# Optimization experiments

Measured on AMD Instinct MI355X. Metric: run time of the kernel, lower is better.

Reference implementation:

```python
import jax, jax.numpy as jnp
import numpy as np

NUM_EMBEDDINGS = 1024
EMBEDDING_DIM = 64
COMMITMENT_COST = 0.25


def setup_inputs() -> dict:
    key = jax.random.key(0)
    k1, k2 = jax.random.split(key)
    inputs = jax.random.normal(k1, (64, 32, 32, EMBEDDING_DIM), dtype=jnp.float32)
    embeddings = jax.random.normal(k2, (NUM_EMBEDDINGS, EMBEDDING_DIM), dtype=jnp.float32)
    return {"inputs": inputs, "embeddings": embeddings}


def reference(inputs, embeddings):
    # flatten spatial dims: [B, HW, D]
    flat = jnp.reshape(inputs, (inputs.shape[0], -1, EMBEDDING_DIM))
    distances = (
        jnp.sum(flat ** 2, axis=2, keepdims=True)
        - 2.0 * jnp.einsum("btd,kd->btk", flat, embeddings)
        + jnp.sum(embeddings ** 2, axis=1)
    )
    encoding_indices = jnp.argmin(distances, axis=2)  # [B, HW]
    # direct gather == one-hot @ embeddings, same math, no [B,HW,K] one-hot
    quantized = jnp.take(embeddings, encoding_indices, axis=0)  # [B, HW, D]
    quantized = jnp.reshape(quantized, inputs.shape)
    e_latent_loss = jnp.mean((jax.lax.stop_gradient(quantized) - inputs) ** 2)
    loss = COMMITMENT_COST * e_latent_loss
    quantized = inputs + jax.lax.stop_gradient(quantized - inputs)
    return quantized, loss, encoding_indices
```

## Files before the change

### kernel.cpp

```cpp
#include <hip/hip_runtime.h>

#define D 64
#define NK 1024
#define QTOTAL 65536
#define NELEM (QTOTAL * D)
#define LOSS_OFF 4194304
#define IDX_OUT_OFF 4194305
#define CAPQ 16384
#define MARGIN 2.0e-3f

typedef float f32x16 __attribute__((ext_vector_type(16)));
typedef short bf16x8 __attribute__((ext_vector_type(8)));
typedef float f32x4 __attribute__((ext_vector_type(4)));
typedef float f32x2 __attribute__((ext_vector_type(2)));
typedef unsigned int u32;
typedef unsigned short ushort_t;

#define WS_E2   0
#define WS_B    4096
#define WS_CNT  266240
#define WS_LIST 266496
#define WS_NEED 332032

__device__ __forceinline__ ushort_t f2bf(float f) {
    u32 u = __float_as_uint(f);
    return (ushort_t)((u + 0x7FFFu + ((u >> 16) & 1u)) >> 16);
}
__device__ __forceinline__ float bf2f(ushort_t h) {
    return __uint_as_float(((u32)h) << 16);
}

__global__ __launch_bounds__(256) void vqk0(const float* __restrict__ emb,
                                            u32* __restrict__ b32,
                                            float* __restrict__ e2, u32* __restrict__ cnt,
                                            float* __restrict__ out) {
    int gid = blockIdx.x * 256 + threadIdx.x;
    int c = gid >> 5;
    int d = (gid & 31) * 2;
    float2 v = ((const float2*)emb)[gid];
    ushort_t h0 = f2bf(v.x), h1 = f2bf(v.y);
    ushort_t m0 = f2bf(v.x - bf2f(h0)), m1 = f2bf(v.y - bf2f(h1));
    int t = c >> 4, row = c & 15;
    int g = (d & 31) >> 3;
    int bh = (d < 32) ? 0 : 1;
    int lane = g * 16 + row;
    int u = t * 1024 + lane * 4 + ((d & 7) >> 1);
    b32[u + bh * 256]       = (u32)h0 | ((u32)h1 << 16);
    b32[u + (bh + 2) * 256] = (u32)m0 | ((u32)m1 << 16);
    if (gid < NK) {
        const float4* e4 = (const float4*)(emb + (long)gid * D);
        float s = 0.f;
#pragma unroll
        for (int i = 0; i < D / 4; ++i) {
            float4 w = e4[i];
            s += w.x * w.x + w.y * w.y + w.z * w.z + w.w * w.w;
        }
        e2[gid] = s;
    }
    if (gid == 0) { out[LOSS_OFF] = 0.0f; *cnt = 0; }
}

#define COMPUTE_TILE(T, BH0, BH1, BM0, BM1) do {                               \
    const int c_ = (T) * 16 + row;                                             \
    const float h_ = e2l[c_];                                                  \
    f32x4 acc = {0.f, 0.f, 0.f, 0.f};                                          \
    acc = __builtin_amdgcn_mfma_f32_16x16x32_bf16(ah[0], BM0, acc, 0, 0, 0);   \
    acc = __builtin_amdgcn_mfma_f32_16x16x32_bf16(am[0], BH0, acc, 0, 0, 0);   \
    acc = __builtin_amdgcn_mfma_f32_16x16x32_bf16(ah[0], BH0, acc, 0, 0, 0);   \
    acc = __builtin_amdgcn_mfma_f32_16x16x32_bf16(ah[1], BM1, acc, 0, 0, 0);   \
    acc = __builtin_amdgcn_mfma_f32_16x16x32_bf16(am[1], BH1, acc, 0, 0, 0);   \
    acc = __builtin_amdgcn_mfma_f32_16x16x32_bf16(ah[1], BH1, acc, 0, 0, 0);   \
    _Pragma("unroll")                                                          \
    for (int r_ = 0; r_ < 4; ++r_) {                                           \
        float sd_ = h_ - acc[r_];                                              \
        float ns2_ = fminf(fmaxf(sd_, s1v[r_]), s2v[r_]);            \
        bool lt_ = sd_ < s1v[r_];                                              \
        i1v[r_] = lt_ ? c_ : i1v[r_];                                          \
        s1v[r_] = fminf(sd_, s1v[r_]);                                         \
        s2v[r_] = ns2_;                                                        \
    }                                                                          \
} while (0)

#define LDS_FRAG(SB, TT, H0, H1, M0, M1) do {                                  \
    const ushort_t* p_ = (SB) + (TT) * 2048 + l * 8;                           \
    H0 = *(const bf16x8*)(p_);                                                 \
    H1 = *(const bf16x8*)(p_ + 512);                                           \
    M0 = *(const bf16x8*)(p_ + 1024);                                          \
    M1 = *(const bf16x8*)(p_ + 1536);                                          \
} while (0)

__global__ __launch_bounds__(512, 4) void vqk1(const float* __restrict__ x,
                                               const ushort_t* __restrict__ B,
                                               const float* __restrict__ e2g,
                                               const float* __restrict__ emb,
                                               u32* __restrict__ cnt,
                                               int* __restrict__ list,
                                               float* __restrict__ out) {
    __shared__ f32x4 stage[2][2048];
    __shared__ float e2l[NK];
    __shared__ int   idx_l[128];
    __shared__ float lred[8];

    const int tid = threadIdx.x;
    const int l = tid & 63;
    const int w = tid >> 6;
    const int qbase = blockIdx.x * 128;
    const int wb = qbase + w * 16;
    const int row = l & 15;
    const int g = l >> 4;
    const int koff = g * 8;

    {
        f32x2 t = ((const f32x2*)e2g)[tid];
        ((f32x2*)e2l)[tid] = t * 0.5f;
    }

    bf16x8 ah[2], am[2];
    {
        const float* xr = x + (long)(wb + row) * D + koff;
#pragma unroll
        for (int half = 0; half < 2; ++half) {
            float4 p0 = ((const float4*)(xr + half * 32))[0];
            float4 p1 = ((const float4*)(xr + half * 32))[1];
            float v[8] = {p0.x, p0.y, p0.z, p0.w, p1.x, p1.y, p1.z, p1.w};
#pragma unroll
            for (int i = 0; i < 8; ++i) {
                ushort_t hs = f2bf(v[i]);
                ushort_t ms = f2bf(v[i] - bf2f(hs));
                ah[half][i] = (short)hs;
                am[half][i] = (short)ms;
            }
        }
    }

    float s1v[4], s2v[4];
    int i1v[4];
#pragma unroll
    for (int i = 0; i < 4; ++i) { s1v[i] = 3.4e38f; s2v[i] = 3.4e38f; i1v[i] = 0; }

    const f32x4* gB = (const f32x4*)B;

    {
        f32x4 st0[4];
#pragma unroll
        for (int tt = 0; tt < 4; ++tt) st0[tt] = gB[tt * 512 + tid];
#pragma unroll
        for (int tt = 0; tt < 4; ++tt) stage[0][tt * 512 + tid] = st0[tt];
    }
    __syncthreads();

#pragma unroll 1
    for (int c = 0; c < 8; ++c) {
        const int cb = c & 1;
        const ushort_t* sb = (const ushort_t*)&stage[cb][0];

        f32x4 st[4];
        if (c < 7) {
#pragma unroll
            for (int tt = 0; tt < 4; ++tt)
                st[tt] = gB[(c + 1) * 2048 + tt * 512 + tid];
        }

        bf16x8 bh0, bh1, bm0, bm1, nh0, nh1, nm0, nm1;
        LDS_FRAG(sb, 0, bh0, bh1, bm0, bm1);
#pragma unroll
        for (int tt = 0; tt < 8; ++tt) {
            if (tt < 7) LDS_FRAG(sb, tt + 1, nh0, nh1, nm0, nm1);
            COMPUTE_TILE(c * 8 + tt, bh0, bh1, bm0, bm1);
            bh0 = nh0; bh1 = nh1; bm0 = nm0; bm1 = nm1;
        }

        if (c < 7) {
#pragma unroll
            for (int tt = 0; tt < 4; ++tt)
                stage[cb ^ 1][tt * 512 + tid] = st[tt];
        }
        __syncthreads();
    }

#pragma unroll
    for (int d = 1; d < 16; d <<= 1) {
#pragma unroll
        for (int sl = 0; sl < 4; ++sl) {
            float os1 = __shfl_xor(s1v[sl], d, 64);
            float os2 = __shfl_xor(s2v[sl], d, 64);
            int   oi1 = __shfl_xor(i1v[sl], d, 64);
            float hi = s1v[sl] > os1 ? s1v[sl] : os1;
            float lo2 = s2v[sl] < os2 ? s2v[sl] : os2;
            int ni = (os1 < s1v[sl]) ? oi1
                   : ((os1 == s1v[sl] && oi1 < i1v[sl]) ? oi1 : i1v[sl]);
            s1v[sl] = s1v[sl] < os1 ? s1v[sl] : os1;
            s2v[sl] = hi < lo2 ? hi : lo2;
            i1v[sl] = ni;
        }
    }

    if (row == 0) {
#pragma unroll
        for (int sl = 0; sl < 4; ++sl) {
            int ql = w * 16 + g * 4 + sl;
            idx_l[ql] = i1v[sl];
            if (s2v[sl] - s1v[sl] <= MARGIN) {
                u32 p = atomicAdd(cnt, 1u);
                if (p < CAPQ) list[p] = qbase + ql;
            }
        }
    }
    __syncthreads();

    if (l < 16) out[IDX_OUT_OFF + wb + l] = (float)idx_l[w * 16 + l];

    const f32x4* x4 = (const f32x4*)(x + (long)wb * D);
    const f32x4* e4 = (const f32x4*)emb;
    f32x4* o4 = (f32x4*)(out + (long)wb * D);
    float ls = 0.f;
#pragma unroll 1
    for (int k = 0; k < 4; ++k) {
        int j = l + 64 * k;
        int ql = j >> 4;
        int col = j & 15;
        int idx = idx_l[w * 16 + ql];
        f32x4 xv = x4[j];
        f32x4 ev = e4[idx * 16 + col];
        o4[j] = ev;
        f32x4 dd = ev - xv;
        ls += dd[0] * dd[0] + dd[1] * dd[1] + dd[2] * dd[2] + dd[3] * dd[3];
    }
#pragma unroll
    for (int offr = 32; offr > 0; offr >>= 1) ls += __shfl_down(ls, offr, 64);
    if (l == 0) lred[w] = ls;
    __syncthreads();
    if (tid == 0) {
        float t = 0.f;
#pragma unroll
        for (int i = 0; i < 8; ++i) t += lred[i];
        atomicAdd(&out[LOSS_OFF], t * (0.25f / (float)NELEM));
    }
}

__global__ __launch_bounds__(64) void vqk2(const float* __restrict__ x,
                                           const float* __restrict__ emb,
                                           const float* __restrict__ e2,
                                           const int* __restrict__ list,
                                           const u32* __restrict__ cnt,
                                           float* __restrict__ out) {
    u32 n = *cnt; if (n > CAPQ) n = CAPQ;
    const int l = threadIdx.x;
    for (u32 f = blockIdx.x; f < n; f += gridDim.x) {
        int q = list[f];
        float4 xv[16];
        const float4* xp = (const float4*)(x + (long)q * D);
#pragma unroll
        for (int i = 0; i < 16; ++i) xv[i] = xp[i];
        float best = 3.4e38f; int bi = 0;
#pragma unroll 1
        for (int i = 0; i < 16; ++i) {
            int c = l * 16 + i;
            const float4* ep = (const float4*)(emb + (long)c * D);
            float a0 = 0.f, a1 = 0.f, a2 = 0.f, a3 = 0.f;
#pragma unroll
            for (int k = 0; k < 16; ++k) {
                float4 e = ep[k];
                a0 = fmaf(e.x, xv[k].x, a0); a1 = fmaf(e.y, xv[k].y, a1);
                a2 = fmaf(e.z, xv[k].z, a2); a3 = fmaf(e.w, xv[k].w, a3);
            }
            float s = 0.5f * e2[c] - ((a0 + a1) + (a2 + a3));
            if (s < best) { best = s; bi = c; }
        }
#pragma unroll
        for (int off = 32; off > 0; off >>= 1) {
            float ob = __shfl_down(best, off, 64);
            int   oi = __shfl_down(bi, off, 64);
            if (ob < best || (ob == best && oi < bi)) { best = ob; bi = oi; }
        }
        bi = __shfl(bi, 0, 64);
        int ci = (int)out[IDX_OUT_OFF + q];
        if (bi != ci) {
            float xl = x[(long)q * D + l];
            float en = emb[(long)bi * D + l];
            float eo = emb[(long)ci * D + l];
            out[(long)q * D + l] = en;
            float dn = (en - xl) * (en - xl);
            float dol = (eo - xl) * (eo - xl);
            float dd = dn - dol;
#pragma unroll
            for (int off = 32; off > 0; off >>= 1) dd += __shfl_down(dd, off, 64);
            if (l == 0) {
                out[IDX_OUT_OFF + q] = (float)bi;
                atomicAdd(&out[LOSS_OFF], dd * (0.25f / (float)NELEM));
            }
        }
    }
}

#define FDO_CHUNK(B, K) \
    aA0 = fmaf(B[0],  xA[4*K+0].x, aA0); aA1 = fmaf(B[1],  xA[4*K+0].y, aA1); \
    aA2 = fmaf(B[2],  xA[4*K+0].z, aA2); aA3 = fmaf(B[3],  xA[4*K+0].w, aA3); \
    aA0 = fmaf(B[4],  xA[4*K+1].x, aA0); aA1 = fmaf(B[5],  xA[4*K+1].y, aA1); \
    aA2 = fmaf(B[6],  xA[4*K+1].z, aA2); aA3 = fmaf(B[7],  xA[4*K+1].w, aA3); \
    aA0 = fmaf(B[8],  xA[4*K+2].x, aA0); aA1 = fmaf(B[9],  xA[4*K+2].y, aA1); \
    aA2 = fmaf(B[10], xA[4*K+2].z, aA2); aA3 = fmaf(B[11], xA[4*K+2].w, aA3); \
    aA0 = fmaf(B[12], xA[4*K+3].x, aA0); aA1 = fmaf(B[13], xA[4*K+3].y, aA1); \
    aA2 = fmaf(B[14], xA[4*K+3].z, aA2); aA3 = fmaf(B[15], xA[4*K+3].w, aA3); \
    aB0 = fmaf(B[0],  xB[4*K+0].x, aB0); aB1 = fmaf(B[1],  xB[4*K+0].y, aB1); \
    aB2 = fmaf(B[2],  xB[4*K+0].z, aB2); aB3 = fmaf(B[3],  xB[4*K+0].w, aB3); \
    aB0 = fmaf(B[4],  xB[4*K+1].x, aB0); aB1 = fmaf(B[5],  xB[4*K+1].y, aB1); \
    aB2 = fmaf(B[6],  xB[4*K+1].z, aB2); aB3 = fmaf(B[7],  xB[4*K+1].w, aB3); \
    aB0 = fmaf(B[8],  xB[4*K+2].x, aB0); aB1 = fmaf(B[9],  xB[4*K+2].y, aB1); \
    aB2 = fmaf(B[10], xB[4*K+2].z, aB2); aB3 = fmaf(B[11], xB[4*K+2].w, aB3); \
    aB0 = fmaf(B[12], xB[4*K+3].x, aB0); aB1 = fmaf(B[13], xB[4*K+3].y, aB1); \
    aB2 = fmaf(B[14], xB[4*K+3].z, aB2); aB3 = fmaf(B[15], xB[4*K+3].w, aB3);

__global__ __launch_bounds__(256) void vq_e2f(const float* __restrict__ emb,
                                              float* __restrict__ e2,
                                              float* __restrict__ out) {
    int k = blockIdx.x * blockDim.x + threadIdx.x;
    if (k == 0) out[LOSS_OFF] = 0.0f;
    if (k < NK) {
        const float4* e4 = (const float4*)(emb + k * D);
        float s = 0.f;
#pragma unroll
        for (int i = 0; i < D / 4; ++i) {
            float4 v = e4[i];
            s += v.x * v.x + v.y * v.y + v.z * v.z + v.w * v.w;
        }
        e2[k] = s;
    }
}

__global__ __launch_bounds__(256, 2) void vq_mainf(const float* __restrict__ x,
                                                   const float* __restrict__ emb,
                                                   const float* __restrict__ e2g,
                                                   float* __restrict__ out) {
    __shared__ float e2l[NK];
    __shared__ float sm_s[512];
    __shared__ int   sm_c[512];
    const int tid = threadIdx.x;
    const int l = tid & 63;
    const int w = tid >> 6;
    const int qbase = blockIdx.x * 128;
    ((float4*)e2l)[tid] = ((const float4*)e2g)[tid];
    float4 xA[16], xB[16];
    const float4* xpA = (const float4*)(x + (long)(qbase + l) * D);
    const float4* xpB = (const float4*)(x + (long)(qbase + 64 + l) * D);
#pragma unroll
    for (int i = 0; i < 16; ++i) { xA[i] = xpA[i]; xB[i] = xpB[i]; }
    __syncthreads();
    const int code0 = __builtin_amdgcn_readfirstlane(w << 8);
    const float* ep0 = emb + (long)code0 * D;
    float bestA = 3.4e38f, bestB = 3.4e38f;
    int idxA = 0, idxB = 0;
#pragma unroll 1
    for (int g = 0; g < 256; ++g) {
        const float* ep = ep0 + g * D;
        f32x16 b0, b1, b2, b3;
        asm volatile(
            "s_load_dwordx16 %0, %4, 0x0\n\t"
            "s_load_dwordx16 %1, %4, 0x40\n\t"
            "s_load_dwordx16 %2, %4, 0x80\n\t"
            "s_load_dwordx16 %3, %4, 0xC0\n\t"
            "s_waitcnt lgkmcnt(0)"
            : "=s"(b0), "=s"(b1), "=s"(b2), "=s"(b3) : "s"(ep));
        float aA0 = 0.f, aA1 = 0.f, aA2 = 0.f, aA3 = 0.f;
        float aB0 = 0.f, aB1 = 0.f, aB2 = 0.f, aB3 = 0.f;
        FDO_CHUNK(b0, 0) FDO_CHUNK(b1, 1) FDO_CHUNK(b2, 2) FDO_CHUNK(b3, 3)
        float dotA = (aA0 + aA1) + (aA2 + aA3);
        float dotB = (aB0 + aB1) + (aB2 + aB3);
        float e2c = e2l[code0 + g];
        float sA = 0.5f * e2c - dotA;
        float sB = 0.5f * e2c - dotB;
        int code = code0 + g;
        bool lt;
        lt = sA < bestA; bestA = lt ? sA : bestA; idxA = lt ? code : idxA;
        lt = sB < bestB; bestB = lt ? sB : bestB; idxB = lt ? code : idxB;
    }
    sm_s[w * 128 + l] = bestA;      sm_c[w * 128 + l] = idxA;
    sm_s[w * 128 + 64 + l] = bestB; sm_c[w * 128 + 64 + l] = idxB;
    __syncthreads();
    if (tid < 128) {
        float bs = sm_s[tid]; int bc = sm_c[tid];
#pragma unroll
        for (int wv = 1; wv < 4; ++wv) {
            float s = sm_s[wv * 128 + tid]; int c = sm_c[wv * 128 + tid];
            if (s < bs) { bs = s; bc = c; }
        }
        const int q = qbase + tid;
        out[IDX_OUT_OFF + q] = (float)bc;
        const float4* eb = (const float4*)(emb + (long)bc * D);
        const float4* xq = (const float4*)(x + (long)q * D);
        float4* oq = (float4*)(out + (long)q * D);
        float lsum = 0.f;
#pragma unroll
        for (int i = 0; i < 16; ++i) {
            float4 e = eb[i]; float4 xx = xq[i];
            oq[i] = e;
            float dx = e.x - xx.x, dy = e.y - xx.y, dz = e.z - xx.z, dw = e.w - xx.w;
            lsum += dx * dx + dy * dy + dz * dz + dw * dw;
        }
#pragma unroll
        for (int o = 32; o > 0; o >>= 1) lsum += __shfl_down(lsum, o, 64);
        if ((tid & 63) == 0) atomicAdd(&out[LOSS_OFF], lsum * (0.25f / (float)NELEM));
    }
}

extern "C" void kernel_launch(void* const* d_in, const int* in_sizes, int n_in,
                              void* d_out, int out_size, void* d_ws, size_t ws_size,
                              hipStream_t stream) {
    const float* x   = (const float*)d_in[0];
    const float* emb = (const float*)d_in[1];
    float* out = (float*)d_out;
    char* ws = (char*)d_ws;

    if (ws_size < (size_t)WS_NEED) {
        float* e2 = (float*)ws;
        vq_e2f<<<4, 256, 0, stream>>>(emb, e2, out);
        vq_mainf<<<QTOTAL / 128, 256, 0, stream>>>(x, emb, e2, out);
        return;
    }

    float* e2    = (float*)(ws + WS_E2);
    ushort_t* B  = (ushort_t*)(ws + WS_B);
    u32* cnt     = (u32*)(ws + WS_CNT);
    int* list    = (int*)(ws + WS_LIST);

    vqk0<<<128, 256, 0, stream>>>(emb, (u32*)B, e2, cnt, out);
    vqk1<<<QTOTAL / 128, 512, 0, stream>>>(x, B, e2, emb, cnt, list, out);
    vqk2<<<256, 64, 0, stream>>>(x, emb, e2, list, cnt, out);
}
```

Before: 121.0 us.

## Stream codebook via direct global-to-LDS loads, halve block size, split MFMA chains

```diff
diff --git a/kernel.cpp b/kernel.cpp
--- a/kernel.cpp
+++ b/kernel.cpp
@@ -12,7 +12,6 @@
 typedef float f32x16 __attribute__((ext_vector_type(16)));
 typedef short bf16x8 __attribute__((ext_vector_type(8)));
 typedef float f32x4 __attribute__((ext_vector_type(4)));
-typedef float f32x2 __attribute__((ext_vector_type(2)));
 typedef unsigned int u32;
 typedef unsigned short ushort_t;
 
@@ -29,6 +28,14 @@
 __device__ __forceinline__ float bf2f(ushort_t h) {
     return __uint_as_float(((u32)h) << 16);
 }
+
+#define GL2LDS(G, L)                                                           \
+    __builtin_amdgcn_global_load_lds(                                          \
+        (const __attribute__((address_space(1))) void*)                        \
+            (unsigned long long)(const void*)(G),                              \
+        (__attribute__((address_space(3))) void*)                              \
+            (unsigned)(unsigned long long)(const void*)(L),                    \
+        16, 0, 0)
 
 __global__ __launch_bounds__(256) void vqk0(const float* __restrict__ emb,
                                             u32* __restrict__ b32,
@@ -63,16 +70,17 @@
 #define COMPUTE_TILE(T, BH0, BH1, BM0, BM1) do {                               \
     const int c_ = (T) * 16 + row;                                             \
     const float h_ = e2l[c_];                                                  \
-    f32x4 acc = {0.f, 0.f, 0.f, 0.f};                                          \
-    acc = __builtin_amdgcn_mfma_f32_16x16x32_bf16(ah[0], BM0, acc, 0, 0, 0);   \
-    acc = __builtin_amdgcn_mfma_f32_16x16x32_bf16(am[0], BH0, acc, 0, 0, 0);   \
-    acc = __builtin_amdgcn_mfma_f32_16x16x32_bf16(ah[0], BH0, acc, 0, 0, 0);   \
-    acc = __builtin_amdgcn_mfma_f32_16x16x32_bf16(ah[1], BM1, acc, 0, 0, 0);   \
-    acc = __builtin_amdgcn_mfma_f32_16x16x32_bf16(am[1], BH1, acc, 0, 0, 0);   \
-    acc = __builtin_amdgcn_mfma_f32_16x16x32_bf16(ah[1], BH1, acc, 0, 0, 0);   \
+    f32x4 a0 = {0.f, 0.f, 0.f, 0.f};                                           \
+    f32x4 a1 = {0.f, 0.f, 0.f, 0.f};                                           \
+    a0 = __builtin_amdgcn_mfma_f32_16x16x32_bf16(ah[0], BM0, a0, 0, 0, 0);     \
+    a1 = __builtin_amdgcn_mfma_f32_16x16x32_bf16(ah[1], BM1, a1, 0, 0, 0);     \
+    a0 = __builtin_amdgcn_mfma_f32_16x16x32_bf16(am[0], BH0, a0, 0, 0, 0);     \
+    a1 = __builtin_amdgcn_mfma_f32_16x16x32_bf16(am[1], BH1, a1, 0, 0, 0);     \
+    a0 = __builtin_amdgcn_mfma_f32_16x16x32_bf16(ah[0], BH0, a0, 0, 0, 0);     \
+    a1 = __builtin_amdgcn_mfma_f32_16x16x32_bf16(ah[1], BH1, a1, 0, 0, 0);     \
     _Pragma("unroll")                                                          \
     for (int r_ = 0; r_ < 4; ++r_) {                                           \
-        float sd_ = h_ - acc[r_];                                              \
+        float sd_ = h_ - a0[r_] - a1[r_];                                      \
         float ns2_ = fminf(fmaxf(sd_, s1v[r_]), s2v[r_]);            \
         bool lt_ = sd_ < s1v[r_];                                              \
         i1v[r_] = lt_ ? c_ : i1v[r_];                                          \
@@ -89,30 +97,35 @@
     M1 = *(const bf16x8*)(p_ + 1536);                                          \
 } while (0)
 
-__global__ __launch_bounds__(512, 4) void vqk1(const float* __restrict__ x,
+__global__ __launch_bounds__(256, 4) void vqk1(const float* __restrict__ x,
                                                const ushort_t* __restrict__ B,
                                                const float* __restrict__ e2g,
                                                const float* __restrict__ emb,
                                                u32* __restrict__ cnt,
                                                int* __restrict__ list,
                                                float* __restrict__ out) {
-    __shared__ f32x4 stage[2][2048];
+    __shared__ f32x4 stage[2][1024];
     __shared__ float e2l[NK];
-    __shared__ int   idx_l[128];
-    __shared__ float lred[8];
+    __shared__ int   idx_l[64];
+    __shared__ float lred[4];
 
     const int tid = threadIdx.x;
     const int l = tid & 63;
     const int w = tid >> 6;
-    const int qbase = blockIdx.x * 128;
+    const int qbase = blockIdx.x * 64;
     const int wb = qbase + w * 16;
     const int row = l & 15;
     const int g = l >> 4;
     const int koff = g * 8;
 
+    const f32x4* gB = (const f32x4*)B;
+
+#pragma unroll
+    for (int tt = 0; tt < 4; ++tt)
+        GL2LDS(gB + tt * 256 + tid, &stage[0][tt * 256 + (tid & 192)]);
     {
-        f32x2 t = ((const f32x2*)e2g)[tid];
-        ((f32x2*)e2l)[tid] = t * 0.5f;
+        f32x4 t = ((const f32x4*)e2g)[tid];
+        ((f32x4*)e2l)[tid] = t * 0.5f;
     }
 
     bf16x8 ah[2], am[2];
@@ -138,42 +151,27 @@
 #pragma unroll
     for (int i = 0; i < 4; ++i) { s1v[i] = 3.4e38f; s2v[i] = 3.4e38f; i1v[i] = 0; }
 
-    const f32x4* gB = (const f32x4*)B;
-
-    {
-        f32x4 st0[4];
-#pragma unroll
-        for (int tt = 0; tt < 4; ++tt) st0[tt] = gB[tt * 512 + tid];
-#pragma unroll
-        for (int tt = 0; tt < 4; ++tt) stage[0][tt * 512 + tid] = st0[tt];
-    }
     __syncthreads();
 
 #pragma unroll 1
-    for (int c = 0; c < 8; ++c) {
+    for (int c = 0; c < 16; ++c) {
         const int cb = c & 1;
         const ushort_t* sb = (const ushort_t*)&stage[cb][0];
 
-        f32x4 st[4];
-        if (c < 7) {
+        if (c < 15) {
 #pragma unroll
             for (int tt = 0; tt < 4; ++tt)
-                st[tt] = gB[(c + 1) * 2048 + tt * 512 + tid];
+                GL2LDS(gB + (c + 1) * 1024 + tt * 256 + tid,
+                       &stage[cb ^ 1][tt * 256 + (tid & 192)]);
         }
 
         bf16x8 bh0, bh1, bm0, bm1, nh0, nh1, nm0, nm1;
         LDS_FRAG(sb, 0, bh0, bh1, bm0, bm1);
 #pragma unroll
-        for (int tt = 0; tt < 8; ++tt) {
-            if (tt < 7) LDS_FRAG(sb, tt + 1, nh0, nh1, nm0, nm1);
-            COMPUTE_TILE(c * 8 + tt, bh0, bh1, bm0, bm1);
+        for (int tt = 0; tt < 4; ++tt) {
+            if (tt < 3) LDS_FRAG(sb, tt + 1, nh0, nh1, nm0, nm1);
+            COMPUTE_TILE(c * 4 + tt, bh0, bh1, bm0, bm1);
             bh0 = nh0; bh1 = nh1; bm0 = nm0; bm1 = nm1;
-        }
-
-        if (c < 7) {
-#pragma unroll
-            for (int tt = 0; tt < 4; ++tt)
-                stage[cb ^ 1][tt * 512 + tid] = st[tt];
         }
         __syncthreads();
     }
@@ -230,12 +228,9 @@
     for (int offr = 32; offr > 0; offr >>= 1) ls += __shfl_down(ls, offr, 64);
     if (l == 0) lred[w] = ls;
     __syncthreads();
-    if (tid == 0) {
-        float t = 0.f;
-#pragma unroll
-        for (int i = 0; i < 8; ++i) t += lred[i];
-        atomicAdd(&out[LOSS_OFF], t * (0.25f / (float)NELEM));
-    }
+    if (tid == 0)
+        atomicAdd(&out[LOSS_OFF],
+                  (lred[0] + lred[1] + lred[2] + lred[3]) * (0.25f / (float)NELEM));
 }
 
 __global__ __launch_bounds__(64) void vqk2(const float* __restrict__ x,
@@ -424,6 +419,6 @@
     int* list    = (int*)(ws + WS_LIST);
 
     vqk0<<<128, 256, 0, stream>>>(emb, (u32*)B, e2, cnt, out);
-    vqk1<<<QTOTAL / 128, 512, 0, stream>>>(x, B, e2, emb, cnt, list, out);
+    vqk1<<<QTOTAL / 64, 256, 0, stream>>>(x, B, e2, emb, cnt, list, out);
     vqk2<<<256, 64, 0, stream>>>(x, emb, e2, list, cnt, out);
 }
```

Result: no change. 123.2 us (+1.9%).
